# Performance work log

Measured on AMD Instinct MI355X. Metric: run time of the kernel, lower is better.

Reference implementation:

```python
import jax, jax.numpy as jnp
import numpy as np

SIZES = [4096, 4096, 4096, 4096]  # input, hidden0, hidden1, output


def setup_inputs() -> dict:
    key = jax.random.key(0)
    ks = jax.random.split(key, 16)
    inp = {"x": jax.random.normal(ks[0], (SIZES[0],), dtype=jnp.float32)}
    ki = 1
    for i in range(3):
        fan_in, fan_out = SIZES[i], SIZES[i + 1]
        bound = 1.0 / np.sqrt(fan_in)
        inp[f"W{i}"] = jax.random.uniform(ks[ki], (fan_out, fan_in), minval=-bound, maxval=bound, dtype=jnp.float32)
        inp[f"b{i}"] = jax.random.uniform(ks[ki + 1], (fan_out,), minval=-bound, maxval=bound, dtype=jnp.float32)
        # hebbian_coeff initialized to ones in __init__, but allow generic values
        inp[f"H{i}"] = jax.random.normal(ks[ki + 2], (fan_out, fan_in, 5), dtype=jnp.float32) * 0.01
        ki += 3
    return inp


def _forward(x, Ws, bs, Hs):
    # MLP forward collecting per-layer activations (states)
    states = [x]
    h = x
    for W, b in zip(Ws[:-1], bs[:-1]):
        h = jnp.tanh(h @ W.T + b)
        states.append(h)
    y = h @ Ws[-1].T + bs[-1]
    states.append(jax.nn.sigmoid(y))  # env_name == 'CartPole-v1'
    # Hebbian ABCD update. NOTE: in the original, delta_weights aliases
    # layer.weight, so every element is overwritten with delta and the
    # subsequent `+=` produces new_weight = 2 * delta (old weight discarded).
    new_Ws = []
    for W, H, pre, post in zip(Ws, Hs, states[:-1], states[1:]):
        A, B, C, D, E = (H[..., m] for m in range(5))  # each [out, in]
        pre_b = pre[None, :]    # [1, in]
        post_b = post[:, None]  # [out, 1]
        delta = A * (B * pre_b * post_b + C * pre_b + D * post_b + E)
        new_Ws.append(2.0 * delta)
    return (y, *new_Ws)


def reference(x, W0, b0, W1, b1, W2, b2, H0, H1, H2):
    return _forward(x, [W0, W1, W2], [b0, b1, b2], [H0, H1, H2])
```

## Files before the change

### kernel.cpp

```cpp
#include <hip/hip_runtime.h>
#include <math.h>

#define N 4096

__global__ __launch_bounds__(256) void mv_kernel(const float* __restrict__ W,
                                                 const float* __restrict__ b,
                                                 const float* __restrict__ x,
                                                 float* __restrict__ out,
                                                 float* __restrict__ out_sig,
                                                 int mode) {
    const int wave = threadIdx.x >> 6;
    const int lane = threadIdx.x & 63;
    const int row  = blockIdx.x * 4 + wave;

    const float4* Wr = reinterpret_cast<const float4*>(W + (size_t)row * N);
    const float4* xv = reinterpret_cast<const float4*>(x);

    float acc = 0.0f;
#pragma unroll
    for (int i = 0; i < 16; ++i) {
        float4 w4 = Wr[lane + i * 64];
        float4 x4 = xv[lane + i * 64];
        acc += w4.x * x4.x;
        acc += w4.y * x4.y;
        acc += w4.z * x4.z;
        acc += w4.w * x4.w;
    }

#pragma unroll
    for (int off = 32; off > 0; off >>= 1)
        acc += __shfl_down(acc, off, 64);

    if (lane == 0) {
        float v = acc + b[row];
        if (mode == 0) {
            out[row] = tanhf(v);
        } else {
            out[row]     = v;
            out_sig[row] = 1.0f / (1.0f + expf(-v));
        }
    }
}

__global__ __launch_bounds__(256) void hebb_kernel(const float* __restrict__ H,
                                                   const float* __restrict__ pre,
                                                   const float* __restrict__ post,
                                                   float* __restrict__ outW) {
    const int idx = blockIdx.x * 256 + threadIdx.x;
    const int p   = idx >> 10;
    const int q0  = (idx & 1023) << 2;

    const size_t base = ((size_t)p * N + q0) * 5;
    const float4* h4  = reinterpret_cast<const float4*>(H + base);
    float4 v0 = h4[0];
    float4 v1 = h4[1];
    float4 v2 = h4[2];
    float4 v3 = h4[3];
    float4 v4 = h4[4];

    const float f[20] = {v0.x, v0.y, v0.z, v0.w,
                         v1.x, v1.y, v1.z, v1.w,
                         v2.x, v2.y, v2.z, v2.w,
                         v3.x, v3.y, v3.z, v3.w,
                         v4.x, v4.y, v4.z, v4.w};

    const float  po = post[p];
    const float4 pr = *reinterpret_cast<const float4*>(pre + q0);
    const float  prs[4] = {pr.x, pr.y, pr.z, pr.w};

    float4 o;
    float* op = &o.x;
#pragma unroll
    for (int k = 0; k < 4; ++k) {
        const float A = f[5 * k + 0];
        const float B = f[5 * k + 1];
        const float C = f[5 * k + 2];
        const float D = f[5 * k + 3];
        const float E = f[5 * k + 4];
        op[k] = 2.0f * A * (B * prs[k] * po + C * prs[k] + D * po + E);
    }

    *reinterpret_cast<float4*>(outW + (size_t)p * N + q0) = o;
}

extern "C" void kernel_launch(void* const* d_in, const int* in_sizes, int n_in,
                              void* d_out, int out_size, void* d_ws, size_t ws_size,
                              hipStream_t stream) {
    const float* x  = (const float*)d_in[0];
    const float* W0 = (const float*)d_in[1];
    const float* b0 = (const float*)d_in[2];
    const float* H0 = (const float*)d_in[3];
    const float* W1 = (const float*)d_in[4];
    const float* b1 = (const float*)d_in[5];
    const float* H1 = (const float*)d_in[6];
    const float* W2 = (const float*)d_in[7];
    const float* b2 = (const float*)d_in[8];
    const float* H2 = (const float*)d_in[9];

    float* out = (float*)d_out;
    float* y   = out;
    float* oW0 = out + N;
    float* oW1 = oW0 + (size_t)N * N;
    float* oW2 = oW1 + (size_t)N * N;

    float* s  = (float*)d_ws;
    float* s1 = s;
    float* s2 = s + N;
    float* s3 = s + 2 * N;

    const dim3 mvGrid(N / 4), mvBlock(256);
    const dim3 hGrid((size_t)N * N / 4 / 256), hBlock(256);

    hipLaunchKernelGGL(mv_kernel, mvGrid, mvBlock, 0, stream, W0, b0, x, s1, (float*)nullptr, 0);
    hipLaunchKernelGGL(hebb_kernel, hGrid, hBlock, 0, stream, H0, x, s1, oW0);

    hipLaunchKernelGGL(mv_kernel, mvGrid, mvBlock, 0, stream, W1, b1, s1, s2, (float*)nullptr, 0);
    hipLaunchKernelGGL(hebb_kernel, hGrid, hBlock, 0, stream, H1, s1, s2, oW1);

    hipLaunchKernelGGL(mv_kernel, mvGrid, mvBlock, 0, stream, W2, b2, s2, y, s3, 1);
    hipLaunchKernelGGL(hebb_kernel, hGrid, hBlock, 0, stream, H2, s2, s3, oW2);
}
```

Baseline: 259.3 us.

## Fuse matvec and Hebbian update into one per-row kernel per layer

Merges each layer's matrix-vector product and Hebbian weight update into a single kernel with one block per output row. The block computes the row's post-activation through a block reduction, then applies the ABCD update over the H row. It issues the first H loads before the reduction so their latency overlaps the dot product. H is read and the new weights are written with nontemporal hints to avoid polluting the cache. This cuts six launches to three and streams W, H and the output within one kernel, at the cost of two block-wide barriers per row.

```diff
diff --git a/kernel.cpp b/kernel.cpp
--- a/kernel.cpp
+++ b/kernel.cpp
@@ -3,84 +3,94 @@
 
 #define N 4096
 
-__global__ __launch_bounds__(256) void mv_kernel(const float* __restrict__ W,
-                                                 const float* __restrict__ b,
-                                                 const float* __restrict__ x,
-                                                 float* __restrict__ out,
-                                                 float* __restrict__ out_sig,
-                                                 int mode) {
-    const int wave = threadIdx.x >> 6;
-    const int lane = threadIdx.x & 63;
-    const int row  = blockIdx.x * 4 + wave;
+typedef float f32x4 __attribute__((ext_vector_type(4)));
 
-    const float4* Wr = reinterpret_cast<const float4*>(W + (size_t)row * N);
-    const float4* xv = reinterpret_cast<const float4*>(x);
+__global__ __launch_bounds__(256) void fused_layer(const float* __restrict__ W,
+                                                   const float* __restrict__ b,
+                                                   const float* __restrict__ H,
+                                                   const float* __restrict__ pre,
+                                                   float* __restrict__ post_out,
+                                                   float* __restrict__ y_out,
+                                                   float* __restrict__ outW,
+                                                   int mode) {
+    const int p   = blockIdx.x;
+    const int tid = threadIdx.x;
 
+    __shared__ float red[4];
+    __shared__ float s_post;
+
+    const f32x4* xv   = reinterpret_cast<const f32x4*>(pre);
+    const float* Hrow = H + (size_t)p * N * 5;
+    float*       Orow = outW + (size_t)p * N;
+
+    const int q0_0 = tid * 4;
+    const f32x4* h4_0 = reinterpret_cast<const f32x4*>(Hrow + (size_t)q0_0 * 5);
+    f32x4 f0 = __builtin_nontemporal_load(h4_0 + 0);
+    f32x4 f1 = __builtin_nontemporal_load(h4_0 + 1);
+    f32x4 f2 = __builtin_nontemporal_load(h4_0 + 2);
+    f32x4 f3 = __builtin_nontemporal_load(h4_0 + 3);
+    f32x4 f4 = __builtin_nontemporal_load(h4_0 + 4);
+    f32x4 pr0 = xv[tid];
+
+    const f32x4* Wr = reinterpret_cast<const f32x4*>(W + (size_t)p * N);
     float acc = 0.0f;
 #pragma unroll
-    for (int i = 0; i < 16; ++i) {
-        float4 w4 = Wr[lane + i * 64];
-        float4 x4 = xv[lane + i * 64];
-        acc += w4.x * x4.x;
-        acc += w4.y * x4.y;
-        acc += w4.z * x4.z;
-        acc += w4.w * x4.w;
+    for (int i = 0; i < 4; ++i) {
+        const int j = tid + i * 256;
+        f32x4 w4 = Wr[j];
+        f32x4 x4 = xv[j];
+        acc += w4.x * x4.x + w4.y * x4.y + w4.z * x4.z + w4.w * x4.w;
+    }
+#pragma unroll
+    for (int off = 32; off > 0; off >>= 1)
+        acc += __shfl_down(acc, off, 64);
+    const int lane = tid & 63;
+    const int wave = tid >> 6;
+    if (lane == 0) red[wave] = acc;
+    __syncthreads();
+    if (tid == 0) {
+        const float v = red[0] + red[1] + red[2] + red[3] + b[p];
+        float post;
+        if (mode == 0) {
+            post = tanhf(v);
+        } else {
+            y_out[p] = v;
+            post = 1.0f / (1.0f + expf(-v));
+        }
+        post_out[p] = post;
+        s_post = post;
+    }
+    __syncthreads();
+    const float po = s_post;
+
+    {
+        f32x4 o;
+        o.x = 2.0f * f0.x * (f0.y * pr0.x * po + f0.z * pr0.x + f0.w * po + f1.x);
+        o.y = 2.0f * f1.y * (f1.z * pr0.y * po + f1.w * pr0.y + f2.x * po + f2.y);
+        o.z = 2.0f * f2.z * (f2.w * pr0.z * po + f3.x * pr0.z + f3.y * po + f3.z);
+        o.w = 2.0f * f3.w * (f4.x * pr0.w * po + f4.y * pr0.w + f4.z * po + f4.w);
+        __builtin_nontemporal_store(o, reinterpret_cast<f32x4*>(Orow + q0_0));
     }
 
 #pragma unroll
-    for (int off = 32; off > 0; off >>= 1)
-        acc += __shfl_down(acc, off, 64);
+    for (int r = 1; r < 4; ++r) {
+        const int g  = tid + r * 256;
+        const int q0 = g * 4;
+        const f32x4* h4 = reinterpret_cast<const f32x4*>(Hrow + (size_t)q0 * 5);
+        f32x4 v0 = __builtin_nontemporal_load(h4 + 0);
+        f32x4 v1 = __builtin_nontemporal_load(h4 + 1);
+        f32x4 v2 = __builtin_nontemporal_load(h4 + 2);
+        f32x4 v3 = __builtin_nontemporal_load(h4 + 3);
+        f32x4 v4 = __builtin_nontemporal_load(h4 + 4);
+        f32x4 pr = xv[g];
 
-    if (lane == 0) {
-        float v = acc + b[row];
-        if (mode == 0) {
-            out[row] = tanhf(v);
-        } else {
-            out[row]     = v;
-            out_sig[row] = 1.0f / (1.0f + expf(-v));
-        }
+        f32x4 o;
+        o.x = 2.0f * v0.x * (v0.y * pr.x * po + v0.z * pr.x + v0.w * po + v1.x);
+        o.y = 2.0f * v1.y * (v1.z * pr.y * po + v1.w * pr.y + v2.x * po + v2.y);
+        o.z = 2.0f * v2.z * (v2.w * pr.z * po + v3.x * pr.z + v3.y * po + v3.z);
+        o.w = 2.0f * v3.w * (v4.x * pr.w * po + v4.y * pr.w + v4.z * po + v4.w);
+        __builtin_nontemporal_store(o, reinterpret_cast<f32x4*>(Orow + q0));
     }
-}
-
-__global__ __launch_bounds__(256) void hebb_kernel(const float* __restrict__ H,
-                                                   const float* __restrict__ pre,
-                                                   const float* __restrict__ post,
-                                                   float* __restrict__ outW) {
-    const int idx = blockIdx.x * 256 + threadIdx.x;
-    const int p   = idx >> 10;
-    const int q0  = (idx & 1023) << 2;
-
-    const size_t base = ((size_t)p * N + q0) * 5;
-    const float4* h4  = reinterpret_cast<const float4*>(H + base);
-    float4 v0 = h4[0];
-    float4 v1 = h4[1];
-    float4 v2 = h4[2];
-    float4 v3 = h4[3];
-    float4 v4 = h4[4];
-
-    const float f[20] = {v0.x, v0.y, v0.z, v0.w,
-                         v1.x, v1.y, v1.z, v1.w,
-                         v2.x, v2.y, v2.z, v2.w,
-                         v3.x, v3.y, v3.z, v3.w,
-                         v4.x, v4.y, v4.z, v4.w};
-
-    const float  po = post[p];
-    const float4 pr = *reinterpret_cast<const float4*>(pre + q0);
-    const float  prs[4] = {pr.x, pr.y, pr.z, pr.w};
-
-    float4 o;
-    float* op = &o.x;
-#pragma unroll
-    for (int k = 0; k < 4; ++k) {
-        const float A = f[5 * k + 0];
-        const float B = f[5 * k + 1];
-        const float C = f[5 * k + 2];
-        const float D = f[5 * k + 3];
-        const float E = f[5 * k + 4];
-        op[k] = 2.0f * A * (B * prs[k] * po + C * prs[k] + D * po + E);
-    }
-
-    *reinterpret_cast<float4*>(outW + (size_t)p * N + q0) = o;
 }
 
 extern "C" void kernel_launch(void* const* d_in, const int* in_sizes, int n_in,
@@ -108,15 +118,9 @@
     float* s2 = s + N;
     float* s3 = s + 2 * N;
 
-    const dim3 mvGrid(N / 4), mvBlock(256);
-    const dim3 hGrid((size_t)N * N / 4 / 256), hBlock(256);
+    const dim3 grid(N), block(256);
 
-    hipLaunchKernelGGL(mv_kernel, mvGrid, mvBlock, 0, stream, W0, b0, x, s1, (float*)nullptr, 0);
-    hipLaunchKernelGGL(hebb_kernel, hGrid, hBlock, 0, stream, H0, x, s1, oW0);
-
-    hipLaunchKernelGGL(mv_kernel, mvGrid, mvBlock, 0, stream, W1, b1, s1, s2, (float*)nullptr, 0);
-    hipLaunchKernelGGL(hebb_kernel, hGrid, hBlock, 0, stream, H1, s1, s2, oW1);
-
-    hipLaunchKernelGGL(mv_kernel, mvGrid, mvBlock, 0, stream, W2, b2, s2, y, s3, 1);
-    hipLaunchKernelGGL(hebb_kernel, hGrid, hBlock, 0, stream, H2, s2, s3, oW2);
+    hipLaunchKernelGGL(fused_layer, grid, block, 0, stream, W0, b0, H0, x,  s1, (float*)nullptr, oW0, 0);
+    hipLaunchKernelGGL(fused_layer, grid, block, 0, stream, W1, b1, H1, s1, s2, (float*)nullptr, oW1, 0);
+    hipLaunchKernelGGL(fused_layer, grid, block, 0, stream, W2, b2, H2, s2, s3, y,               oW2, 1);
 }
```

Result: slower. 409.7 us (+58.0%).
